# Kernel tuning notes

Measured on AMD Instinct MI355X. Metric: run time of the kernel, lower is better.

## Reference

```python
import jax, jax.numpy as jnp
import numpy as np

DECAY = 0.99
EPS = 1e-6


def setup_inputs() -> dict:
    key = jax.random.key(0)
    k1, k2, k3, k4 = jax.random.split(key, 4)
    B, L, D, K = 32, 1024, 512, 8192
    return {
        "z_e": jax.random.normal(k1, (B, L, D), dtype=jnp.float32),
        "codebook": jax.random.normal(k2, (K, D), dtype=jnp.float32),
        "cluster_size": jax.random.uniform(k3, (K,), dtype=jnp.float32),
        "ema_w": jax.random.normal(k4, (K, D), dtype=jnp.float32),
    }


def reference(z_e, codebook, cluster_size, ema_w):
    B, L, D = z_e.shape
    K = codebook.shape[0]
    flat = z_e.reshape(-1, D)  # [N, D], N = B*L

    dist = ((flat * flat).sum(1, keepdims=True)
            - 2.0 * flat @ codebook.T
            + (codebook * codebook).sum(1))
    idx = jnp.argmin(dist, axis=1)  # [N]
    z_q = codebook[idx].reshape(B, L, D)

    # EMA statistics (training-mode buffer update); one-hot scatter -> segment_sum
    counts = jax.ops.segment_sum(jnp.ones((B * L,), flat.dtype), idx, num_segments=K)
    dw = jax.ops.segment_sum(flat, idx, num_segments=K)  # [K, D]
    new_cluster_size = DECAY * cluster_size + (1.0 - DECAY) * counts
    new_ema_w = DECAY * ema_w + (1.0 - DECAY) * dw
    n = new_cluster_size.sum()
    cs = (new_cluster_size + EPS) / (n + K * EPS) * n  # Laplace-smoothed counts
    new_codebook = new_ema_w / cs[:, None]

    # loss = mse(sg(z_q), z_e) + 0.25 * mse(z_e, sg(z_q)) = 1.25 * mse
    zq_sg = jax.lax.stop_gradient(z_q)
    loss = 1.25 * jnp.mean((z_e - zq_sg) ** 2)

    # straight-through estimator
    z_q_st = z_e + jax.lax.stop_gradient(z_q - z_e)
    return z_q_st, idx.reshape(B, L), loss, new_codebook, new_cluster_size, new_ema_w
```

## Files before the change

### kernel.cpp

```cpp
#include <hip/hip_runtime.h>


constexpr int N = 32768;
constexpr int D = 512;
constexpr int K = 8192;
constexpr int CAP  = 8192;
constexpr int CAPE = 4096;

constexpr float DECAYF  = 0.99f;
constexpr float OMDECAY = (float)(1.0 - 0.99);
constexpr float EPSF    = 1e-6f;
constexpr float KEPSF   = (float)(8192 * 1e-6);
constexpr float TAU1    = 0.7f;
constexpr float TAU2    = 0.005f;

typedef unsigned int       u32;
typedef unsigned short     u16;
typedef unsigned long long u64;
typedef float  f32x4 __attribute__((ext_vector_type(4)));
typedef u32    u32x4 __attribute__((ext_vector_type(4)));
typedef __bf16 bf16x8 __attribute__((ext_vector_type(8)));

#define AS1 __attribute__((address_space(1)))
#define AS3 __attribute__((address_space(3)))

constexpr size_t OFF_CNORM  = 0;
constexpr size_t OFF_IDX    = OFF_CNORM + K;
constexpr size_t OFF_CNTI   = OFF_IDX + N;
constexpr size_t OFF_FLAGC  = OFF_CNTI + K;
constexpr size_t OFF_FLAG2C = OFF_FLAGC + 1;
constexpr size_t OFF_NEXT   = OFF_FLAG2C + 1;
constexpr size_t OFF_OFFS   = OFF_NEXT + K;
constexpr size_t OFF_LIST   = OFF_OFFS + K + 1;
constexpr size_t OFF_FLAGL  = OFF_LIST + N;
constexpr size_t OFF_FLAG2L = OFF_FLAGL + CAP;
constexpr size_t OFF_PB1    = OFF_FLAG2L + N;
constexpr size_t OFF_PB2    = OFF_PB1 + 16 * CAP;
constexpr size_t OFF_PI1    = OFF_PB2 + 16 * CAP;
constexpr size_t OFF_ESLOT  = (OFF_PI1 + 16 * CAP + 1) & ~(size_t)1;
constexpr size_t OFF_SUMS   = (OFF_ESLOT + 2 * CAPE + 1) & ~(size_t)1;
constexpr size_t OFF_LOSSP  = (OFF_SUMS + 2 + 1) & ~(size_t)1;
constexpr size_t OFF_CBH    = (OFF_LOSSP + 2 * K + 3) & ~(size_t)3;
static_assert((OFF_ESLOT & 1) == 0 && (OFF_SUMS & 1) == 0 && (OFF_LOSSP & 1) == 0, "align");
static_assert((OFF_CBH & 3) == 0, "16B align");

constexpr size_t OUT_ZQ   = 0;
constexpr size_t OUT_IDX  = OUT_ZQ + (size_t)N * D;
constexpr size_t OUT_LOSS = OUT_IDX + N;
constexpr size_t OUT_NCB  = OUT_LOSS + 1;
constexpr size_t OUT_NCS  = OUT_NCB + (size_t)K * D;
constexpr size_t OUT_EMA  = OUT_NCS + K;
constexpr size_t XH_F  = OUT_ZQ;
constexpr size_t PX2_F = OUT_ZQ + (size_t)N * 256;
constexpr size_t PB1H_F = OUT_EMA;
constexpr size_t PB2H_F = OUT_EMA + 4 * (size_t)N;
constexpr size_t PI1H_F = OUT_EMA + 8 * (size_t)N;

__device__ inline u16 f32_to_bf16_rne(float f)
{
    u32 u = __builtin_bit_cast(u32, f);
    u = (u + 0x7FFFu + ((u >> 16) & 1u)) >> 16;
    return (u16)u;
}

__global__ __launch_bounds__(256) void split_hi_kernel(const float* __restrict__ src,
                                                       u32x4* __restrict__ dst)
{
    const int T = blockIdx.x;
    const int w = threadIdx.x >> 6;
    const int l = threadIdx.x & 63;
    const int row = T * 16 + (l & 15);
#pragma unroll
    for (int i = 0; i < 4; ++i) {
        const int S  = w * 4 + i;
        const int q4 = S * 8 + (l >> 4) * 2;
        const float4 va = ((const float4*)src)[(size_t)row * 128 + q4];
        const float4 vb = ((const float4*)src)[(size_t)row * 128 + q4 + 1];
        const float a[8] = {va.x, va.y, va.z, va.w, vb.x, vb.y, vb.z, vb.w};
        u32x4 o;
#pragma unroll
        for (int j = 0; j < 4; ++j)
            ((u32*)&o)[j] = (u32)f32_to_bf16_rne(a[2 * j]) |
                            ((u32)f32_to_bf16_rne(a[2 * j + 1]) << 16);
        dst[((size_t)T * 16 + S) * 64 + l] = o;
    }
}

__global__ __launch_bounds__(256) void cbprep_kernel(const float* __restrict__ cb,
                                                     u32x4* __restrict__ CBH,
                                                     u32x4* __restrict__ CB2,
                                                     float* __restrict__ cnorm)
{
    const int T = blockIdx.x;
    const int w = threadIdx.x >> 6;
    const int l = threadIdx.x & 63;
    {
        const int row = T * 16 + (l & 15);
#pragma unroll
        for (int i = 0; i < 4; ++i) {
            const int S  = w * 4 + i;
            const int q4 = S * 8 + (l >> 4) * 2;
            const float4 va = ((const float4*)cb)[(size_t)row * 128 + q4];
            const float4 vb = ((const float4*)cb)[(size_t)row * 128 + q4 + 1];
            const float a[8] = {va.x, va.y, va.z, va.w, vb.x, vb.y, vb.z, vb.w};
            u32x4 o;
#pragma unroll
            for (int j = 0; j < 4; ++j)
                ((u32*)&o)[j] = (u32)f32_to_bf16_rne(a[2 * j]) |
                                ((u32)f32_to_bf16_rne(a[2 * j + 1]) << 16);
            CBH[((size_t)T * 16 + S) * 64 + l] = o;
        }
    }
    {
        const int row = T * 16 + (l & 15);
        const int cq  = l >> 4;
#pragma unroll
        for (int i = 0; i < 8; ++i) {
            const int S = w + 4 * i;
            const float4 v = ((const float4*)cb)[(size_t)row * 128 + S * 4 + cq];
            u32x4 o;
            const float a[4] = {v.x, v.y, v.z, v.w};
#pragma unroll
            for (int j = 0; j < 4; ++j) {
                const u16 hi = f32_to_bf16_rne(a[j]);
                const float hif = __builtin_bit_cast(float, (u32)hi << 16);
                const u16 lo = f32_to_bf16_rne(a[j] - hif);
                ((u32*)&o)[j] = (u32)hi | ((u32)lo << 16);
            }
            CB2[((size_t)T * 32 + S) * 64 + l] = o;
        }
    }
#pragma unroll
    for (int sub = 0; sub < 4; ++sub) {
        const int row = T * 16 + sub * 4 + w;
        const float4* r = (const float4*)(cb + (size_t)row * D);
        const float4 v0 = r[l];
        const float4 v1 = r[l + 64];
        float s = v0.x * v0.x + v0.y * v0.y + v0.z * v0.z + v0.w * v0.w
                + v1.x * v1.x + v1.y * v1.y + v1.z * v1.z + v1.w * v1.w;
#pragma unroll
        for (int m = 32; m >= 1; m >>= 1) s += __shfl_xor(s, m, 64);
        if (l == 0) cnorm[row] = s;
    }
}

__global__ __launch_bounds__(256) void repack_kernel(
    const float* __restrict__ z_e, const int* __restrict__ flag_cnt,
    const int* __restrict__ flag_list, u32x4* __restrict__ PX2)
{
    const int B = blockIdx.x;
    const int cnt = min(*flag_cnt, CAP);
    if (B * 16 >= cnt) return;
    const int w = threadIdx.x >> 6;
    const int l = threadIdx.x & 63;
    const int srow = B * 16 + (l & 15);
    const int n = (srow < cnt) ? (flag_list[srow] & (N - 1)) : 0;
    const int cq = l >> 4;
#pragma unroll
    for (int i = 0; i < 8; ++i) {
        const int S = w + 4 * i;
        const float4 v = ((const float4*)z_e)[(size_t)n * 128 + S * 4 + cq];
        u32x4 o;
        const float a[4] = {v.x, v.y, v.z, v.w};
#pragma unroll
        for (int j = 0; j < 4; ++j) {
            const u16 hi = f32_to_bf16_rne(a[j]);
            const float hif = __builtin_bit_cast(float, (u32)hi << 16);
            const u16 lo = f32_to_bf16_rne(a[j] - hif);
            ((u32*)&o)[j] = (u32)hi | ((u32)lo << 16);
        }
        PX2[((size_t)B * 32 + S) * 64 + l] = o;
    }
}

constexpr int BPH = 128, BCH = 512, KIH = 32;
constexpr int NSTEPH = 16;
constexpr int NCHQ   = 4;
constexpr int TOTQ   = NCHQ * NSTEPH;
constexpr int CELH = BCH * KIH;
constexpr int XELH = BPH * KIH;
constexpr int BUFH = CELH + XELH;

__global__ __launch_bounds__(512, 2) void argmin_hi_kernel(
    const u16* __restrict__ CBH, const u16* __restrict__ XH,
    const float* __restrict__ cnorm,
    float* __restrict__ pb1h, float* __restrict__ pb2h, int* __restrict__ pi1h)
{
    __shared__ __align__(16) u16 lds[2][BUFH];

    const int b    = blockIdx.x;
    const int kq   = (b & 7) >> 1;
    const int n0   = ((b >> 3) * 2 + (b & 1)) * BPH;
    const int tid  = threadIdx.x;
    const int w    = tid >> 6;
    const int lane = tid & 63;
    const int lhi  = lane >> 4;

    u32 cbo[4], xo;
#pragma unroll
    for (int m = 0; m < 4; ++m) {
        const int flat = m * 512 + tid;
        cbo[m] = (u32)(kq * 1048576 + (flat >> 6) * 8192 + (flat & 63) * 8);
    }
    xo = (u32)((n0 / 16 + (tid >> 6)) * 8192 + (tid & 63) * 8);

    auto stage = [&](int parity) {
        u16* bufp = &lds[parity][0];
#pragma unroll
        for (int m = 0; m < 4; ++m) {
            __builtin_amdgcn_global_load_lds((const AS1 u32*)(CBH + cbo[m]),
                (AS3 u32*)(bufp + (m * 512 + tid) * 8), 16, 0, 0);
            cbo[m] += 512;
        }
        __builtin_amdgcn_global_load_lds((const AS1 u32*)(XH + xo),
            (AS3 u32*)(bufp + CELH + tid * 8), 16, 0, 0);
        xo += 512;
    };

    float b1[8], b2[8]; int i1[8];
#pragma unroll
    for (int p = 0; p < 8; ++p) { b1[p] = INFINITY; b2[p] = INFINITY; i1[p] = 0; }

    stage(0);
    __syncthreads();
    int sc = 1;

    for (int cc = 0; cc < NCHQ; ++cc) {
        f32x4 acc[4][8];
        const f32x4 zero = {0.f, 0.f, 0.f, 0.f};
#pragma unroll
        for (int cg = 0; cg < 4; ++cg)
#pragma unroll
            for (int p = 0; p < 8; ++p) acc[cg][p] = zero;

        for (int s8 = 0; s8 < NSTEPH; ++s8) {
            const u16* cur = &lds[s8 & 1][0];
            if (sc < TOTQ) {
                if ((sc & (NSTEPH - 1)) == 0) {
#pragma unroll
                    for (int m = 0; m < 4; ++m) cbo[m] += 262144 - 8192;
                    xo -= 8192;
                }
                stage(sc & 1);
                ++sc;
            }
            u32x4 bfr[8];
#pragma unroll
            for (int p = 0; p < 8; ++p)
                bfr[p] = *(const u32x4*)(cur + CELH + p * 512 + lane * 8);
#pragma unroll
            for (int cg = 0; cg < 4; ++cg) {
                const u32x4 af = *(const u32x4*)(cur + (w * 4 + cg) * 512 + lane * 8);
#pragma unroll
                for (int p = 0; p < 8; ++p)
                    acc[cg][p] = __builtin_amdgcn_mfma_f32_16x16x32_bf16(
                        __builtin_bit_cast(bf16x8, af),
                        __builtin_bit_cast(bf16x8, bfr[p]), acc[cg][p], 0, 0, 0);
            }
            __syncthreads();
        }

        const int gchunk = kq * NCHQ + cc;
        const int cb0 = gchunk * BCH + w * 64;
#pragma unroll
        for (int cg = 0; cg < 4; ++cg) {
            const int code0 = cb0 + cg * 16 + lhi * 4;
            const float4 cn4 = *(const float4*)(cnorm + code0);
            const float cn[4] = {cn4.x, cn4.y, cn4.z, cn4.w};
#pragma unroll
            for (int p = 0; p < 8; ++p) {
                const f32x4 A = acc[cg][p];
                const float dv[4] = {cn[0] - 2.f * A.x, cn[1] - 2.f * A.y,
                                     cn[2] - 2.f * A.z, cn[3] - 2.f * A.w};
#pragma unroll
                for (int r = 0; r < 4; ++r) {
                    if (dv[r] < b1[p]) { b2[p] = b1[p]; b1[p] = dv[r]; i1[p] = code0 + r; }
                    else if (dv[r] < b2[p]) { b2[p] = dv[r]; }
                }
            }
        }
    }

#pragma unroll
    for (int p = 0; p < 8; ++p) {
#pragma unroll
        for (int m = 16; m <= 32; m <<= 1) {
            const float ob1 = __shfl_xor(b1[p], m, 64);
            const float ob2 = __shfl_xor(b2[p], m, 64);
            const int   oi1 = __shfl_xor(i1[p], m, 64);
            const float nb2 = fminf(fminf(b2[p], ob2), fmaxf(b1[p], ob1));
            if (ob1 < b1[p] || (ob1 == b1[p] && oi1 < i1[p])) { b1[p] = ob1; i1[p] = oi1; }
            b2[p] = nb2;
        }
    }

    __syncthreads();

    float* mb1 = (float*)&lds[0][0];
    float* mb2 = mb1 + 8 * BPH;
    int*   mi  = (int*)(mb2 + 8 * BPH);
    if (lane < 16) {
#pragma unroll
        for (int p = 0; p < 8; ++p) {
            const int pt = p * 16 + lane;
            mb1[w * BPH + pt] = b1[p];
            mb2[w * BPH + pt] = b2[p];
            mi [w * BPH + pt] = i1[p];
        }
    }
    __syncthreads();
    if (tid < BPH) {
        float fb1 = INFINITY, fb2 = INFINITY; int fi = 0;
        for (int ww = 0; ww < 8; ++ww) {
            const float a1 = mb1[ww * BPH + tid], a2 = mb2[ww * BPH + tid];
            const int   ai = mi[ww * BPH + tid];
            const float nb2 = fminf(fminf(fb2, a2), fmaxf(fb1, a1));
            if (a1 < fb1 || (a1 == fb1 && ai < fi)) { fb1 = a1; fi = ai; }
            fb2 = nb2;
        }
        const int n = n0 + tid;
        pb1h[kq * N + n] = fb1;
        pb2h[kq * N + n] = fb2;
        pi1h[kq * N + n] = fi;
    }
}

__global__ __launch_bounds__(256) void merge_hi_kernel(
    const float* __restrict__ pb1h, const float* __restrict__ pb2h,
    const int* __restrict__ pi1h,
    int* __restrict__ idx_i, float* __restrict__ idx_f,
    int* __restrict__ flag_cnt, int* __restrict__ flag_list,
    int* __restrict__ flag2_cnt, int* __restrict__ flag2_list)
{
    const int n = blockIdx.x * 256 + threadIdx.x;
    float fb1 = INFINITY, fb2 = INFINITY; int fi = 0x7fffffff;
#pragma unroll
    for (int q = 0; q < 4; ++q) {
        const float a1 = pb1h[q * N + n], a2 = pb2h[q * N + n];
        const int   ai = pi1h[q * N + n];
        const float nb2 = fminf(fminf(fb2, a2), fmaxf(fb1, a1));
        if (a1 < fb1 || (a1 == fb1 && ai < fi)) { fb1 = a1; fi = ai; }
        fb2 = nb2;
    }
    idx_i[n] = fi;
    idx_f[n] = (float)fi;
    if (fb2 - fb1 < TAU1) {
        const int pos = atomicAdd(flag_cnt, 1);
        if (pos < CAP) flag_list[pos] = n;
        else {
            const int p2 = atomicAdd(flag2_cnt, 1);
            if ((unsigned)p2 < (unsigned)N) flag2_list[p2] = n;
        }
    }
}

constexpr int CEL2 = 512 * 32;
constexpr int XEL2 = 128 * 32;
constexpr int BUF2 = CEL2 + XEL2;

__global__ __launch_bounds__(512, 2) void argmin_part_kernel(
    const u16* __restrict__ CB2, const u16* __restrict__ PX2,
    const float* __restrict__ cnorm, const int* __restrict__ flag_cnt,
    float* __restrict__ pb1, float* __restrict__ pb2, int* __restrict__ pi1)
{
    const int q  = blockIdx.x & 15;
    const int sb = blockIdx.x >> 4;
    const int cnt = min(*flag_cnt, CAP);
    if (sb * 128 >= cnt) return;
    const int n0s = sb * 128;

    __shared__ __align__(16) u16 lds[2][BUF2];

    const int tid  = threadIdx.x;
    const int w    = tid >> 6;
    const int lane = tid & 63;
    const int lhi  = lane >> 4;

    auto stage = [&](u16* bufp, int s) {
#pragma unroll
        for (int j = 0; j < 4; ++j) {
            const int slot = j * 512 + tid;
            const u16* gsrc = CB2 + (((size_t)(q * 32 + (slot >> 6)) * 32 + s) * 512
                                     + (slot & 63) * 8);
            __builtin_amdgcn_global_load_lds((const AS1 u32*)gsrc,
                                             (AS3 u32*)(bufp + slot * 8), 16, 0, 0);
        }
        const u16* gx = PX2 + (((size_t)(n0s / 16 + (tid >> 6)) * 32 + s) * 512
                               + (tid & 63) * 8);
        __builtin_amdgcn_global_load_lds((const AS1 u32*)gx,
                                         (AS3 u32*)(bufp + CEL2 + tid * 8), 16, 0, 0);
    };

    float b1[8], b2[8]; int i1[8];
#pragma unroll
    for (int p = 0; p < 8; ++p) { b1[p] = INFINITY; b2[p] = INFINITY; i1[p] = 0; }

    f32x4 acc[4][8];
    const f32x4 zero = {0.f, 0.f, 0.f, 0.f};
#pragma unroll
    for (int cg = 0; cg < 4; ++cg)
#pragma unroll
        for (int p = 0; p < 8; ++p) acc[cg][p] = zero;

    stage(&lds[0][0], 0);
    __syncthreads();

#pragma unroll 2
    for (int s = 0; s < 32; ++s) {
        const u16* cur = (s & 1) ? &lds[1][0] : &lds[0][0];
        u16* nxt       = (s & 1) ? &lds[0][0] : &lds[1][0];
        if (s + 1 < 32) stage(nxt, s + 1);

        u32x4 bfr[8];
#pragma unroll
        for (int p = 0; p < 8; ++p)
            bfr[p] = *(const u32x4*)(cur + CEL2 + p * 512 + lane * 8);
#pragma unroll
        for (int cg = 0; cg < 4; ++cg) {
            const u32x4 af = *(const u32x4*)(cur + (w * 4 + cg) * 512 + lane * 8);
            u32x4 as;
            as.x = (af.x >> 16) | (af.x << 16);
            as.y = (af.y >> 16) | (af.y << 16);
            as.z = (af.z >> 16) | (af.z << 16);
            as.w = (af.w >> 16) | (af.w << 16);
#pragma unroll
            for (int p = 0; p < 8; ++p) {
                acc[cg][p] = __builtin_amdgcn_mfma_f32_16x16x32_bf16(
                    __builtin_bit_cast(bf16x8, af), __builtin_bit_cast(bf16x8, bfr[p]),
                    acc[cg][p], 0, 0, 0);
                acc[cg][p] = __builtin_amdgcn_mfma_f32_16x16x32_bf16(
                    __builtin_bit_cast(bf16x8, as), __builtin_bit_cast(bf16x8, bfr[p]),
                    acc[cg][p], 0, 0, 0);
            }
        }
        __syncthreads();
    }

    const int cb0 = q * 512 + w * 64;
#pragma unroll
    for (int cg = 0; cg < 4; ++cg) {
        const int code0 = cb0 + cg * 16 + lhi * 4;
        const float4 cn4 = *(const float4*)(cnorm + code0);
        const float cn[4] = {cn4.x, cn4.y, cn4.z, cn4.w};
#pragma unroll
        for (int p = 0; p < 8; ++p) {
            const f32x4 A = acc[cg][p];
            const float dv[4] = {cn[0] - 2.f * A.x, cn[1] - 2.f * A.y,
                                 cn[2] - 2.f * A.z, cn[3] - 2.f * A.w};
#pragma unroll
            for (int r = 0; r < 4; ++r) {
                if (dv[r] < b1[p]) { b2[p] = b1[p]; b1[p] = dv[r]; i1[p] = code0 + r; }
                else if (dv[r] < b2[p]) { b2[p] = dv[r]; }
            }
        }
    }

#pragma unroll
    for (int p = 0; p < 8; ++p) {
#pragma unroll
        for (int m = 16; m <= 32; m <<= 1) {
            const float ob1 = __shfl_xor(b1[p], m, 64);
            const float ob2 = __shfl_xor(b2[p], m, 64);
            const int   oi1 = __shfl_xor(i1[p], m, 64);
            const float nb2 = fminf(fminf(b2[p], ob2), fmaxf(b1[p], ob1));
            if (ob1 < b1[p] || (ob1 == b1[p] && oi1 < i1[p])) { b1[p] = ob1; i1[p] = oi1; }
            b2[p] = nb2;
        }
    }

    __syncthreads();

    float* mb1 = (float*)&lds[0][0];
    float* mb2 = mb1 + 8 * 128;
    int*   mi  = (int*)(mb2 + 8 * 128);
    if (lane < 16) {
#pragma unroll
        for (int p = 0; p < 8; ++p) {
            const int pt = p * 16 + lane;
            mb1[w * 128 + pt] = b1[p];
            mb2[w * 128 + pt] = b2[p];
            mi [w * 128 + pt] = i1[p];
        }
    }
    __syncthreads();
    if (tid < 128) {
        float fb1 = INFINITY, fb2 = INFINITY; int fi = 0;
        for (int ww = 0; ww < 8; ++ww) {
            const float a1 = mb1[ww * 128 + tid], a2 = mb2[ww * 128 + tid];
            const int   ai = mi[ww * 128 + tid];
            const float nb2 = fminf(fminf(fb2, a2), fmaxf(fb1, a1));
            if (a1 < fb1 || (a1 == fb1 && ai < fi)) { fb1 = a1; fi = ai; }
            fb2 = nb2;
        }
        const int slot = n0s + tid;
        pb1[q * CAP + slot] = fb1;
        pb2[q * CAP + slot] = fb2;
        pi1[q * CAP + slot] = fi;
    }
}

__global__ __launch_bounds__(256) void combine_kernel(
    const int* __restrict__ flag_cnt, const int* __restrict__ flag_list,
    const float* __restrict__ pb1, const float* __restrict__ pb2,
    const int* __restrict__ pi1,
    int* __restrict__ idx_i, float* __restrict__ idx_f,
    int* __restrict__ flag2_cnt, int* __restrict__ flag2_list)
{
    const int s = blockIdx.x * 256 + threadIdx.x;
    const int cnt = min(*flag_cnt, CAP);
    if (s >= cnt) return;
    float fb1 = INFINITY, fb2 = INFINITY; int fi = 0x7fffffff;
#pragma unroll
    for (int q = 0; q < 16; ++q) {
        const float a1 = pb1[q * CAP + s], a2 = pb2[q * CAP + s];
        const int   ai = pi1[q * CAP + s];
        const float nb2 = fminf(fminf(fb2, a2), fmaxf(fb1, a1));
        if (a1 < fb1 || (a1 == fb1 && ai < fi)) { fb1 = a1; fi = ai; }
        fb2 = nb2;
    }
    const int n = flag_list[s] & (N - 1);
    idx_i[n] = fi;
    idx_f[n] = (float)fi;
    if (fb2 - fb1 < TAU2) {
        const int p2 = atomicAdd(flag2_cnt, 1);
        if ((unsigned)p2 < (unsigned)N) flag2_list[p2] = n;
    }
}

__global__ __launch_bounds__(256) void exact_part_kernel(
    const float* __restrict__ x, const float* __restrict__ cb,
    const float* __restrict__ cnorm, const int* __restrict__ flag2_cnt,
    const int* __restrict__ flag2_list, u64* __restrict__ eslot)
{
    __shared__ float4 xs[128];
    __shared__ u64 red[256];
    const int cnt = min(*flag2_cnt, CAPE);
    const int nwork = cnt * 16;
    for (int j = blockIdx.x; j < nwork; j += gridDim.x) {
        const int s = j >> 4;
        const int q = j & 15;
        const int n = flag2_list[s] & (N - 1);
        __syncthreads();
        if (threadIdx.x < 128)
            xs[threadIdx.x] = ((const float4*)(x + (size_t)n * D))[threadIdx.x];
        __syncthreads();
        u64 bestp = ~0ull;
#pragma unroll
        for (int c = 0; c < 2; ++c) {
            const int k = q * 512 + c * 256 + threadIdx.x;
            const float4* crow = (const float4*)(cb + (size_t)k * D);
            float a0 = 0.f, a1 = 0.f, a2 = 0.f, a3 = 0.f;
            for (int d = 0; d < 128; ++d) {
                const float4 xv = xs[d], cv = crow[d];
                a0 = fmaf(xv.x, cv.x, a0);
                a1 = fmaf(xv.y, cv.y, a1);
                a2 = fmaf(xv.z, cv.z, a2);
                a3 = fmaf(xv.w, cv.w, a3);
            }
            const float dist = cnorm[k] - 2.0f * ((a0 + a1) + (a2 + a3));
            u32 ub = __builtin_bit_cast(u32, dist);
            ub = (ub & 0x80000000u) ? ~ub : (ub | 0x80000000u);
            const u64 pk = ((u64)ub << 32) | (u32)k;
            bestp = bestp < pk ? bestp : pk;
        }
        red[threadIdx.x] = bestp;
        __syncthreads();
        for (int off = 128; off > 0; off >>= 1) {
            if (threadIdx.x < off) {
                const u64 o = red[threadIdx.x + off];
                if (o < red[threadIdx.x]) red[threadIdx.x] = o;
            }
            __syncthreads();
        }
        if (threadIdx.x == 0) atomicMin(&eslot[s], red[0]);
    }
}

__global__ __launch_bounds__(256) void exact_write_kernel(
    const int* __restrict__ flag2_cnt, const int* __restrict__ flag2_list,
    const u64* __restrict__ eslot, int* __restrict__ idx_i, float* __restrict__ idx_f)
{
    const int s = blockIdx.x * 256 + threadIdx.x;
    const int cnt = min(*flag2_cnt, CAPE);
    if (s >= cnt) return;
    const int n = flag2_list[s] & (N - 1);
    const int k = (int)(eslot[s] & (u64)(K - 1));
    idx_i[n] = k;
    idx_f[n] = (float)k;
}

__global__ __launch_bounds__(256) void count_kernel(
    const int* __restrict__ idx_i, int* __restrict__ cnti)
{
    const int p = blockIdx.x * 256 + threadIdx.x;
    atomicAdd(&cnti[idx_i[p] & (K - 1)], 1);
}

__global__ __launch_bounds__(256) void scan_kernel(
    const int* __restrict__ cnti, const float* __restrict__ csz,
    int* __restrict__ offs, int* __restrict__ nxt,
    float* __restrict__ ncs, double* __restrict__ n_sum)
{
    __shared__ int    tsum[256];
    __shared__ double dsum[256];
    const int t = threadIdx.x;
    const int base = t * 32;
    int s = 0;
    double dn = 0.0;
#pragma unroll
    for (int i = 0; i < 32; ++i) {
        const int c = cnti[base + i];
        s += c;
        const float v = DECAYF * csz[base + i] + OMDECAY * (float)c;
        ncs[base + i] = v;
        dn += (double)v;
    }
    tsum[t] = s; dsum[t] = dn;
    __syncthreads();
    int run = 0;
    for (int j = 0; j < t; ++j) run += tsum[j];
#pragma unroll
    for (int i = 0; i < 32; ++i) {
        offs[base + i] = run;
        nxt[base + i] = run;
        run += cnti[base + i];
    }
    if (t == 255) offs[K] = run;
    if (t == 0) {
        double tot = 0.0;
        for (int j = 0; j < 256; ++j) tot += dsum[j];
        n_sum[0] = tot;
    }
}

__global__ __launch_bounds__(256) void fill_kernel(
    const int* __restrict__ idx_i, int* __restrict__ nxt, int* __restrict__ list)
{
    const int p = blockIdx.x * 256 + threadIdx.x;
    const int k = idx_i[p] & (K - 1);
    const int pos = atomicAdd(&nxt[k], 1);
    if ((unsigned)pos < (unsigned)N) list[pos] = p;
}

__global__ __launch_bounds__(128) void gather_finalize_kernel(
    const float* __restrict__ x, const float* __restrict__ cb,
    const int* __restrict__ offs, const int* __restrict__ list,
    const float* __restrict__ ema_w, const float* __restrict__ ncs,
    const double* __restrict__ n_sum, float* __restrict__ new_ema,
    float* __restrict__ new_cb, float* __restrict__ zq,
    double* __restrict__ loss_part)
{
    const int k = blockIdx.x;
    const int t = threadIdx.x;
    const int beg = min(offs[k], N), end = min(offs[k + 1], N);
    const size_t o = (size_t)k * 128 + t;
    const float4 c = ((const float4*)cb)[o];
    float4 acc = {0.f, 0.f, 0.f, 0.f};
    float lsum = 0.f;
    for (int i = beg; i < end; ++i) {
        const int p = list[i] & (N - 1);
        const float4 v = ((const float4*)x)[(size_t)p * 128 + t];
        acc.x += v.x; acc.y += v.y; acc.z += v.z; acc.w += v.w;
        ((float4*)zq)[(size_t)p * 128 + t] = c;
        const float d0 = v.x - c.x, d1 = v.y - c.y, d2 = v.z - c.z, d3 = v.w - c.w;
        lsum += d0 * d0 + d1 * d1 + d2 * d2 + d3 * d3;
    }
    const float n = (float)n_sum[0];
    const float csm = (ncs[k] + EPSF) / (n + KEPSF) * n;
    const float4 e = ((const float4*)ema_w)[o];
    float4 ne;
    ne.x = DECAYF * e.x + OMDECAY * acc.x;
    ne.y = DECAYF * e.y + OMDECAY * acc.y;
    ne.z = DECAYF * e.z + OMDECAY * acc.z;
    ne.w = DECAYF * e.w + OMDECAY * acc.w;
    ((float4*)new_ema)[o] = ne;
    float4 nc;
    nc.x = ne.x / csm; nc.y = ne.y / csm; nc.z = ne.z / csm; nc.w = ne.w / csm;
    ((float4*)new_cb)[o] = nc;

#pragma unroll
    for (int m = 32; m >= 1; m >>= 1) lsum += __shfl_xor(lsum, m, 64);
    __shared__ float prt[2];
    if ((t & 63) == 0) prt[t >> 6] = lsum;
    __syncthreads();
    if (t == 0) loss_part[k] = (double)(prt[0] + prt[1]);
}

__global__ __launch_bounds__(256) void loss_reduce_kernel(
    const double* __restrict__ loss_part, float* __restrict__ out_loss)
{
    __shared__ double red[256];
    const int t = threadIdx.x;
    double s = 0.0;
    for (int i = t; i < K; i += 256) s += loss_part[i];
    red[t] = s;
    __syncthreads();
    for (int off = 128; off > 0; off >>= 1) {
        if (t < off) red[t] += red[t + off];
        __syncthreads();
    }
    if (t == 0)
        out_loss[0] = (float)(1.25 * (red[0] / (double)((size_t)N * D)));
}

extern "C" void kernel_launch(void* const* d_in, const int* in_sizes, int n_in,
                              void* d_out, int out_size, void* d_ws, size_t ws_size,
                              hipStream_t stream)
{
    const float* z_e   = (const float*)d_in[0];
    const float* cbook = (const float*)d_in[1];
    const float* csz   = (const float*)d_in[2];
    const float* ema_w = (const float*)d_in[3];

    float* out = (float*)d_out;
    u32*   ws  = (u32*)d_ws;

    float*  cnorm      = (float*)(ws + OFF_CNORM);
    int*    idx_i      = (int*)(ws + OFF_IDX);
    int*    cnti       = (int*)(ws + OFF_CNTI);
    int*    flag_cnt   = (int*)(ws + OFF_FLAGC);
    int*    flag2_cnt  = (int*)(ws + OFF_FLAG2C);
    int*    nxt        = (int*)(ws + OFF_NEXT);
    int*    offs       = (int*)(ws + OFF_OFFS);
    int*    list       = (int*)(ws + OFF_LIST);
    int*    flag_list  = (int*)(ws + OFF_FLAGL);
    int*    flag2_list = (int*)(ws + OFF_FLAG2L);
    float*  pb1        = (float*)(ws + OFF_PB1);
    float*  pb2        = (float*)(ws + OFF_PB2);
    int*    pi1        = (int*)(ws + OFF_PI1);
    u64*    eslot      = (u64*)(ws + OFF_ESLOT);
    double* n_sum      = (double*)(ws + OFF_SUMS);
    double* loss_part  = (double*)(ws + OFF_LOSSP);
    u16*    CBH        = (u16*)(ws + OFF_CBH);

    u16* XH  = (u16*)(out + XH_F);
    u16* PX2 = (u16*)(out + PX2_F);
    u16* CB2 = (u16*)(out + OUT_NCB);
    float* pb1h = out + PB1H_F;
    float* pb2h = out + PB2H_F;
    int*   pi1h = (int*)(out + PI1H_F);

    hipMemsetAsync(ws + OFF_CNTI, 0, (K + 2) * sizeof(u32), stream);
    hipMemsetAsync(ws + OFF_ESLOT, 0xFF, CAPE * sizeof(u64), stream);

    split_hi_kernel<<<N / 16, 256, 0, stream>>>(z_e, (u32x4*)XH);
    cbprep_kernel<<<K / 16, 256, 0, stream>>>(cbook, (u32x4*)CBH, (u32x4*)CB2, cnorm);

    argmin_hi_kernel<<<(N / BPH) * 4, 512, 0, stream>>>(CBH, XH, cnorm,
                                                        pb1h, pb2h, pi1h);

    merge_hi_kernel<<<N / 256, 256, 0, stream>>>(pb1h, pb2h, pi1h, idx_i,
                                                 out + OUT_IDX, flag_cnt, flag_list,
                                                 flag2_cnt, flag2_list);

    repack_kernel<<<CAP / 16, 256, 0, stream>>>(z_e, flag_cnt, flag_list, (u32x4*)PX2);

    argmin_part_kernel<<<(CAP / 128) * 16, 512, 0, stream>>>(CB2, PX2, cnorm, flag_cnt,
                                                             pb1, pb2, pi1);

    combine_kernel<<<CAP / 256, 256, 0, stream>>>(flag_cnt, flag_list, pb1, pb2, pi1,
                                                  idx_i, out + OUT_IDX,
                                                  flag2_cnt, flag2_list);

    exact_part_kernel<<<2048, 256, 0, stream>>>(z_e, cbook, cnorm, flag2_cnt,
                                                flag2_list, eslot);

    exact_write_kernel<<<CAPE / 256, 256, 0, stream>>>(flag2_cnt, flag2_list, eslot,
                                                       idx_i, out + OUT_IDX);

    count_kernel<<<N / 256, 256, 0, stream>>>(idx_i, cnti);

    scan_kernel<<<1, 256, 0, stream>>>(cnti, csz, offs, nxt, out + OUT_NCS, n_sum);

    fill_kernel<<<N / 256, 256, 0, stream>>>(idx_i, nxt, list);

    gather_finalize_kernel<<<K, 128, 0, stream>>>(z_e, cbook, offs, list, ema_w,
                                                  out + OUT_NCS, n_sum,
                                                  out + OUT_EMA, out + OUT_NCB,
                                                  out + OUT_ZQ, loss_part);

    loss_reduce_kernel<<<1, 256, 0, stream>>>(loss_part, out + OUT_LOSS);
}
```

Before: 754.8 us.

## Reshape argmin tile to 256 points by 256 codes with 2x4 wave grid

Changes the hi-precision argmin GEMM block tile from 128 points x 512 codes to 256 points x 256 codes. Waves are now arranged as 2 point-groups by 4 code-groups instead of all sharing the same points, and the cross-wave reduction is adjusted to match. Each block now handles twice as many points and walks the codebook in twice as many chunks. The square tile is meant to balance LDS traffic between codebook and input fragments and halve the number of blocks that re-read each codebook slice. The cost is double the per-block input staging and more chunk epilogues per block.

```diff
diff --git a/kernel.cpp b/kernel.cpp
--- a/kernel.cpp
+++ b/kernel.cpp
@@ -173,9 +173,9 @@
     }
 }
 
-constexpr int BPH = 128, BCH = 512, KIH = 32;
+constexpr int BPH = 256, BCH = 256, KIH = 32;
 constexpr int NSTEPH = 16;
-constexpr int NCHQ   = 4;
+constexpr int NCHQ   = 8;
 constexpr int TOTQ   = NCHQ * NSTEPH;
 constexpr int CELH = BCH * KIH;
 constexpr int XELH = BPH * KIH;
@@ -193,28 +193,31 @@
     const int n0   = ((b >> 3) * 2 + (b & 1)) * BPH;
     const int tid  = threadIdx.x;
     const int w    = tid >> 6;
+    const int wp   = w >> 2;
+    const int wc   = w & 3;
     const int lane = tid & 63;
     const int lhi  = lane >> 4;
 
-    u32 cbo[4], xo;
-#pragma unroll
-    for (int m = 0; m < 4; ++m) {
+    u32 cbo[2], xo[2];
+#pragma unroll
+    for (int m = 0; m < 2; ++m) {
         const int flat = m * 512 + tid;
-        cbo[m] = (u32)(kq * 1048576 + (flat >> 6) * 8192 + (flat & 63) * 8);
-    }
-    xo = (u32)((n0 / 16 + (tid >> 6)) * 8192 + (tid & 63) * 8);
+        const int g = flat >> 6, li = flat & 63;
+        cbo[m] = (u32)((kq * 128 + g) * 8192 + li * 8);
+        xo[m]  = (u32)((n0 / 16 + g) * 8192 + li * 8);
+    }
 
     auto stage = [&](int parity) {
         u16* bufp = &lds[parity][0];
 #pragma unroll
-        for (int m = 0; m < 4; ++m) {
+        for (int m = 0; m < 2; ++m) {
             __builtin_amdgcn_global_load_lds((const AS1 u32*)(CBH + cbo[m]),
                 (AS3 u32*)(bufp + (m * 512 + tid) * 8), 16, 0, 0);
             cbo[m] += 512;
-        }
-        __builtin_amdgcn_global_load_lds((const AS1 u32*)(XH + xo),
-            (AS3 u32*)(bufp + CELH + tid * 8), 16, 0, 0);
-        xo += 512;
+            __builtin_amdgcn_global_load_lds((const AS1 u32*)(XH + xo[m]),
+                (AS3 u32*)(bufp + CELH + (m * 512 + tid) * 8), 16, 0, 0);
+            xo[m] += 512;
+        }
     };
 
     float b1[8], b2[8]; int i1[8];
@@ -238,8 +241,10 @@
             if (sc < TOTQ) {
                 if ((sc & (NSTEPH - 1)) == 0) {
 #pragma unroll
-                    for (int m = 0; m < 4; ++m) cbo[m] += 262144 - 8192;
-                    xo -= 8192;
+                    for (int m = 0; m < 2; ++m) {
+                        cbo[m] += 16 * 8192 - 8192;
+                        xo[m]  -= 8192;
+                    }
                 }
                 stage(sc & 1);
                 ++sc;
@@ -247,10 +252,10 @@
             u32x4 bfr[8];
 #pragma unroll
             for (int p = 0; p < 8; ++p)
-                bfr[p] = *(const u32x4*)(cur + CELH + p * 512 + lane * 8);
+                bfr[p] = *(const u32x4*)(cur + CELH + (wp * 8 + p) * 512 + lane * 8);
 #pragma unroll
             for (int cg = 0; cg < 4; ++cg) {
-                const u32x4 af = *(const u32x4*)(cur + (w * 4 + cg) * 512 + lane * 8);
+                const u32x4 af = *(const u32x4*)(cur + (wc * 4 + cg) * 512 + lane * 8);
 #pragma unroll
                 for (int p = 0; p < 8; ++p)
                     acc[cg][p] = __builtin_amdgcn_mfma_f32_16x16x32_bf16(
@@ -260,8 +265,7 @@
             __syncthreads();
         }
 
-        const int gchunk = kq * NCHQ + cc;
-        const int cb0 = gchunk * BCH + w * 64;
+        const int cb0 = kq * 2048 + cc * 256 + wc * 64;
 #pragma unroll
         for (int cg = 0; cg < 4; ++cg) {
             const int code0 = cb0 + cg * 16 + lhi * 4;
@@ -297,23 +301,26 @@
     __syncthreads();
 
     float* mb1 = (float*)&lds[0][0];
-    float* mb2 = mb1 + 8 * BPH;
-    int*   mi  = (int*)(mb2 + 8 * BPH);
+    float* mb2 = mb1 + 8 * 128;
+    int*   mi  = (int*)(mb2 + 8 * 128);
     if (lane < 16) {
 #pragma unroll
         for (int p = 0; p < 8; ++p) {
             const int pt = p * 16 + lane;
-            mb1[w * BPH + pt] = b1[p];
-            mb2[w * BPH + pt] = b2[p];
-            mi [w * BPH + pt] = i1[p];
+            mb1[w * 128 + pt] = b1[p];
+            mb2[w * 128 + pt] = b2[p];
+            mi [w * 128 + pt] = i1[p];
         }
     }
     __syncthreads();
     if (tid < BPH) {
+        const int wp2 = tid >> 7;
+        const int pt  = tid & 127;
         float fb1 = INFINITY, fb2 = INFINITY; int fi = 0;
-        for (int ww = 0; ww < 8; ++ww) {
-            const float a1 = mb1[ww * BPH + tid], a2 = mb2[ww * BPH + tid];
-            const int   ai = mi[ww * BPH + tid];
+        for (int ww = 0; ww < 4; ++ww) {
+            const int src = (wp2 * 4 + ww) * 128 + pt;
+            const float a1 = mb1[src], a2 = mb2[src];
+            const int   ai = mi[src];
             const float nb2 = fminf(fminf(fb2, a2), fmaxf(fb1, a1));
             if (a1 < fb1 || (a1 == fb1 && ai < fi)) { fb1 = a1; fi = ai; }
             fb2 = nb2;
```

Measured after the change: 745.1 us. About the same (-1.3%).
